# Kernel optimization log

Measured on AMD Instinct MI355X. Metric: run time of the kernel, lower is better.

The kernel has to match this reference:

```python
import jax, jax.numpy as jnp
import numpy as np

B, S, D, H = 8, 2048, 1024, 8
HD = D // H


def _linear_params(key, d_in, d_out):
    kw, kb = jax.random.split(key)
    w = jax.random.normal(kw, (d_out, d_in), jnp.float32) * 0.02
    b = jax.random.normal(kb, (d_out,), jnp.float32) * 0.02
    return w, b


def setup_inputs() -> dict:
    key = jax.random.key(0)
    ks = jax.random.split(key, 16)
    inp = {}
    inp['input_seq'] = jax.random.normal(ks[0], (B, S, D), jnp.float32)
    inp['output_seq'] = jax.random.normal(ks[1], (B, S, D), jnp.float32)
    # PositionalEncoding parameter: sin(arange(D) / 10000 ** (arange(D)/D))
    ar = jnp.arange(D, dtype=jnp.float32)
    inp['pe'] = jnp.sin(ar / 10000.0 ** (ar / D))
    names = ['enc_wq enc_bq', 'enc_wk enc_bk', 'enc_wv enc_bv',
             'enc_w1 enc_b1', 'enc_w2 enc_b2',
             'dec_s_wq dec_s_bq', 'dec_s_wk dec_s_bk', 'dec_s_wv dec_s_bv',
             'dec_c_wq dec_c_bq', 'dec_c_wk dec_c_bk', 'dec_c_wv dec_c_bv',
             'dec_w1 dec_b1', 'dec_w2 dec_b2', 'fc_w fc_b']
    for i, pair in enumerate(names):
        wn, bn = pair.split()
        w, b = _linear_params(ks[2 + i], D, D)
        inp[wn], inp[bn] = w, b
    return inp


def _mha(q_in, k_in, wq, bq, wk, bk, wv, bv):
    # Faithful to source: head split WITHOUT transpose -> per-position 8x8 head mixing.
    q = (q_in @ wq.T + bq).reshape(q_in.shape[0], q_in.shape[1], H, HD)
    k = (k_in @ wk.T + bk).reshape(k_in.shape[0], k_in.shape[1], H, HD)
    v = (k_in @ wv.T + bv).reshape(k_in.shape[0], k_in.shape[1], H, HD)
    scores = jnp.einsum('bsih,bsjh->bsij', q, k) / jnp.sqrt(jnp.float32(HD))
    w = jax.nn.softmax(scores, axis=-1)  # dropout before softmax is identity at eval
    out = jnp.einsum('bsij,bsjh->bsih', w, v)
    return out.reshape(q_in.shape[0], q_in.shape[1], -1)


def reference(input_seq, output_seq, pe,
              enc_wq, enc_bq, enc_wk, enc_bk, enc_wv, enc_bv,
              enc_w1, enc_b1, enc_w2, enc_b2,
              dec_s_wq, dec_s_bq, dec_s_wk, dec_s_bk, dec_s_wv, dec_s_bv,
              dec_c_wq, dec_c_bq, dec_c_wk, dec_c_bk, dec_c_wv, dec_c_bv,
              dec_w1, dec_b1, dec_w2, dec_b2, fc_w, fc_b):
    x = input_seq + pe  # additive positional encoding
    # encoder layer
    a = _mha(x, x, enc_wq, enc_bq, enc_wk, enc_bk, enc_wv, enc_bv)
    enc_out = jax.nn.relu(a @ enc_w1.T + enc_b1) @ enc_w2.T + enc_b2
    # decoder layer (training branch: output_seq given)
    sa = _mha(output_seq, output_seq, dec_s_wq, dec_s_bq, dec_s_wk, dec_s_bk, dec_s_wv, dec_s_bv)
    ca = _mha(sa, enc_out, dec_c_wq, dec_c_bq, dec_c_wk, dec_c_bk, dec_c_wv, dec_c_bv)
    dec_out = jax.nn.relu(ca @ dec_w1.T + dec_b1) @ dec_w2.T + dec_b2
    return dec_out @ fc_w.T + fc_b
```

## Files before the change

kernel.cpp:

```cpp
#include <hip/hip_runtime.h>
#include <stdint.h>


#define TOKENS 16384
#define DMODEL 1024

typedef unsigned short ushort_t;
typedef __attribute__((ext_vector_type(8))) short short8;
typedef __attribute__((ext_vector_type(4))) float floatx4;

__device__ __forceinline__ float b2f(ushort_t u) {
  union { uint32_t i; float f; } v; v.i = ((uint32_t)u) << 16; return v.f;
}
__device__ __forceinline__ ushort_t f2b(float f) {
  union { float f; uint32_t i; } v; v.f = f;
  uint32_t r = v.i + 0x7fffu + ((v.i >> 16) & 1u);
  return (ushort_t)(r >> 16);
}

__device__ __forceinline__ void pack8(const float* __restrict__ g, ushort_t* dst) {
  float4 x = *(const float4*)g;
  float4 y = *(const float4*)(g + 4);
  ushort_t o[8] = {f2b(x.x), f2b(x.y), f2b(x.z), f2b(x.w),
                   f2b(y.x), f2b(y.y), f2b(y.z), f2b(y.w)};
  *(uint4*)dst = *(uint4*)o;
}

#define GLD16(g, l)                                                          \
  __builtin_amdgcn_global_load_lds(                                          \
      (const __attribute__((address_space(1))) void*)(g),                    \
      (__attribute__((address_space(3))) void*)(l), 16, 0, 0)

struct ConvArgs {
  const float* src[14];
  ushort_t* dst[14];
};

__global__ __launch_bounds__(256) void conv_w_kernel(ConvArgs a) {
  const int w = blockIdx.y;
  const int idx = (blockIdx.x * 256 + threadIdx.x) * 8;
  pack8(a.src[w] + idx, a.dst[w] + idx);
}

__global__ __launch_bounds__(256) void conv_x_kernel(
    const float* __restrict__ src, ushort_t* __restrict__ dst) {
  const int idx = (blockIdx.x * 256 + threadIdx.x) * 8;
  pack8(src + idx, dst + idx);
}

__global__ __launch_bounds__(256) void add_pe_kernel(
    const float* __restrict__ in, const float* __restrict__ pe,
    ushort_t* __restrict__ out) {
  int idx = (blockIdx.x * 256 + threadIdx.x) * 8;
  int d = idx & (DMODEL - 1);
  float4 a0 = *(const float4*)(in + idx);
  float4 a1 = *(const float4*)(in + idx + 4);
  float4 p0 = *(const float4*)(pe + d);
  float4 p1 = *(const float4*)(pe + d + 4);
  ushort_t o[8] = {f2b(a0.x + p0.x), f2b(a0.y + p0.y), f2b(a0.z + p0.z), f2b(a0.w + p0.w),
                   f2b(a1.x + p1.x), f2b(a1.y + p1.y), f2b(a1.z + p1.z), f2b(a1.w + p1.w)};
  *(uint4*)(out + idx) = *(uint4*)o;
}

template <bool RELU, bool OUT32>
__global__ __launch_bounds__(256) void gemm_bt(
    const ushort_t* __restrict__ A, const ushort_t* __restrict__ W,
    const float* __restrict__ bias, void* __restrict__ Cp) {
  constexpr int K = 1024, N = 1024, BK = 64;
  __shared__ __align__(16) ushort_t smem[128 * 136];
  ushort_t* sA = smem;
  ushort_t* sB = smem + 8192;

  const int t = threadIdx.x;
  const int lane = t & 63;
  const int m0 = blockIdx.x * 128;
  const int n0 = blockIdx.y * 128;
  const int wm = ((t >> 6) >> 1) * 64;
  const int wn = ((t >> 6) & 1) * 64;

  floatx4 acc[4][4] = {};

  const int rl = t >> 3;
  const int j8 = t & 7;
  const ushort_t* gA = A + (size_t)(m0 + rl) * K + ((j8 ^ (rl & 7)) * 8);
  const ushort_t* gW = W + (size_t)(n0 + rl) * K + ((j8 ^ (rl & 7)) * 8);
  const int lo = t * 8;

  for (int k0 = 0; k0 < K; k0 += BK) {
#pragma unroll
    for (int s = 0; s < 4; s++) {
      GLD16(gA + k0 + (size_t)(s * 32) * K, sA + s * 2048 + lo);
      GLD16(gW + k0 + (size_t)(s * 32) * K, sB + s * 2048 + lo);
    }
    __syncthreads();

#pragma unroll
    for (int ks = 0; ks < 2; ks++) {
      short8 af[4], bf[4];
#pragma unroll
      for (int i = 0; i < 4; i++) {
        const int cs = ((ks * 4 + (lane >> 4)) ^ (lane & 7)) * 8;
        af[i] = *(const short8*)&sA[(wm + i * 16 + (lane & 15)) * 64 + cs];
        bf[i] = *(const short8*)&sB[(wn + i * 16 + (lane & 15)) * 64 + cs];
      }
#pragma unroll
      for (int i = 0; i < 4; i++)
#pragma unroll
        for (int jj = 0; jj < 4; jj++)
          acc[i][jj] = __builtin_amdgcn_mfma_f32_16x16x32_bf16(af[i], bf[jj], acc[i][jj], 0, 0, 0);
    }
    __syncthreads();
  }

  const int rbase = (lane >> 4) * 4;

  if (OUT32) {
    float* sCf = (float*)smem;
#pragma unroll
    for (int p = 0; p < 2; p++) {
      if (wm == p * 64) {
#pragma unroll
        for (int j = 0; j < 4; j++) {
          const int cl = wn + j * 16 + (lane & 15);
          const float bv = bias[n0 + cl];
#pragma unroll
          for (int i = 0; i < 4; i++)
#pragma unroll
            for (int r = 0; r < 4; r++) {
              float v = acc[i][j][r] + bv;
              if (RELU) v = fmaxf(v, 0.0f);
              sCf[(i * 16 + rbase + r) * 132 + cl] = v;
            }
        }
      }
      __syncthreads();
#pragma unroll
      for (int u = 0; u < 8; u++) {
        const int lin = u * 256 + t;
        const int row = lin >> 5;
        const int cc = (lin & 31) * 4;
        float4 v = *(const float4*)&sCf[row * 132 + cc];
        *(float4*)((float*)Cp + (size_t)(m0 + p * 64 + row) * N + n0 + cc) = v;
      }
      __syncthreads();
    }
    return;
  }

  ushort_t* sC = smem;
#pragma unroll
  for (int j = 0; j < 4; j++) {
    const int cl = wn + j * 16 + (lane & 15);
    const float bv = bias[n0 + cl];
#pragma unroll
    for (int i = 0; i < 4; i++) {
      const int rl2 = wm + i * 16 + rbase;
#pragma unroll
      for (int r = 0; r < 4; r++) {
        float v = acc[i][j][r] + bv;
        if (RELU) v = fmaxf(v, 0.0f);
        sC[(rl2 + r) * 136 + cl] = f2b(v);
      }
    }
  }
  __syncthreads();
#pragma unroll
  for (int p = 0; p < 8; p++) {
    const int rl2 = p * 16 + (t >> 4);
    const int cl = (t & 15) * 8;
    uint4 v = *(const uint4*)&sC[rl2 * 136 + cl];
    *(uint4*)((ushort_t*)Cp + (size_t)(m0 + rl2) * N + n0 + cl) = v;
  }
}

__global__ __launch_bounds__(256) void attn_kernel(
    const ushort_t* Q, const ushort_t* Kp, const ushort_t* Vp, ushort_t* O) {
  __shared__ __align__(16) ushort_t sq[4][1024];
  __shared__ __align__(16) ushort_t sk[4][1024];
  __shared__ __align__(16) ushort_t sv[4][1024];
  __shared__ float sp[4][64];

  const int t = threadIdx.x;
  const int w = t >> 6;
  const int lane = t & 63;
  const size_t base = ((size_t)blockIdx.x * 4 + w) * 1024;

  ((uint4*)sq[w])[lane] = ((const uint4*)(Q + base))[lane];
  ((uint4*)sq[w])[lane + 64] = ((const uint4*)(Q + base))[lane + 64];
  ((uint4*)sk[w])[lane] = ((const uint4*)(Kp + base))[lane];
  ((uint4*)sk[w])[lane + 64] = ((const uint4*)(Kp + base))[lane + 64];
  ((uint4*)sv[w])[lane] = ((const uint4*)(Vp + base))[lane];
  ((uint4*)sv[w])[lane + 64] = ((const uint4*)(Vp + base))[lane + 64];
  __syncthreads();

  {
    const int i = lane >> 3, j = lane & 7;
    const ushort_t* qr = &sq[w][i * 128];
    const ushort_t* kr = &sk[w][j * 128];
    float s = 0.0f;
#pragma unroll 16
    for (int h = 0; h < 128; h++) s += b2f(qr[h]) * b2f(kr[h]);
    s *= 0.08838834764831845f;
    float m = s;
#pragma unroll
    for (int off = 1; off < 8; off <<= 1) m = fmaxf(m, __shfl_xor(m, off, 64));
    float e = __expf(s - m);
    float sum = e;
#pragma unroll
    for (int off = 1; off < 8; off <<= 1) sum += __shfl_xor(sum, off, 64);
    sp[w][lane] = e / sum;
  }
  __syncthreads();

  {
    const int i = lane >> 3;
    const int hb = (lane & 7) * 16;
    float p[8];
#pragma unroll
    for (int jj = 0; jj < 8; jj++) p[jj] = sp[w][i * 8 + jj];
    float o[16];
#pragma unroll
    for (int h = 0; h < 16; h++) {
      float acc = 0.0f;
#pragma unroll
      for (int jj = 0; jj < 8; jj++) acc += p[jj] * b2f(sv[w][jj * 128 + hb + h]);
      o[h] = acc;
    }
    uint32_t packed[8];
#pragma unroll
    for (int u = 0; u < 8; u++)
      packed[u] = (uint32_t)f2b(o[2 * u]) | ((uint32_t)f2b(o[2 * u + 1]) << 16);
    uint4* dst = (uint4*)(O + base + i * 128 + hb);
    dst[0] = *(uint4*)&packed[0];
    dst[1] = *(uint4*)&packed[4];
  }
}

extern "C" void kernel_launch(void* const* d_in, const int* in_sizes, int n_in,
                              void* d_out, int out_size, void* d_ws, size_t ws_size,
                              hipStream_t stream) {
  const float* input_seq = (const float*)d_in[0];
  const float* output_seq = (const float*)d_in[1];
  const float* pe = (const float*)d_in[2];
  const float* wsrc[14] = {
      (const float*)d_in[3],  (const float*)d_in[5],  (const float*)d_in[7],
      (const float*)d_in[9],  (const float*)d_in[11], (const float*)d_in[13],
      (const float*)d_in[15], (const float*)d_in[17], (const float*)d_in[19],
      (const float*)d_in[21], (const float*)d_in[23], (const float*)d_in[25],
      (const float*)d_in[27], (const float*)d_in[29]};
  const float* enc_bq = (const float*)d_in[4];
  const float* enc_bk = (const float*)d_in[6];
  const float* enc_bv = (const float*)d_in[8];
  const float* enc_b1 = (const float*)d_in[10];
  const float* enc_b2 = (const float*)d_in[12];
  const float* dsq_b = (const float*)d_in[14];
  const float* dsk_b = (const float*)d_in[16];
  const float* dsv_b = (const float*)d_in[18];
  const float* dcq_b = (const float*)d_in[20];
  const float* dck_b = (const float*)d_in[22];
  const float* dcv_b = (const float*)d_in[24];
  const float* dec_b1 = (const float*)d_in[26];
  const float* dec_b2 = (const float*)d_in[28];
  const float* fc_b = (const float*)d_in[30];

  const size_t SZ = (size_t)TOKENS * DMODEL;
  const size_t WSZ = (size_t)DMODEL * DMODEL;
  ushort_t* bA = (ushort_t*)d_ws;
  ushort_t* bB = bA + SZ;
  ushort_t* oseq = bB + SZ;
  ushort_t* wts = oseq + SZ;
  ushort_t* oL = (ushort_t*)d_out;
  ushort_t* oH = oL + SZ;
  float* outf = (float*)d_out;

  ConvArgs ca;
#pragma unroll
  for (int i = 0; i < 14; i++) { ca.src[i] = wsrc[i]; ca.dst[i] = wts + (size_t)i * WSZ; }

  const dim3 gG(TOKENS / 128, DMODEL / 128);
  const dim3 blk(256);
  const int gPE = TOKENS * DMODEL / (256 * 8);
  const int gAT = TOKENS / 4;

  conv_w_kernel<<<dim3(WSZ / (256 * 8), 14), blk, 0, stream>>>(ca);
  conv_x_kernel<<<gPE, blk, 0, stream>>>(output_seq, oseq);
  add_pe_kernel<<<gPE, blk, 0, stream>>>(input_seq, pe, bA);
  gemm_bt<false, false><<<gG, blk, 0, stream>>>(bA, wts + 0 * WSZ, enc_bq, bB);
  gemm_bt<false, false><<<gG, blk, 0, stream>>>(bA, wts + 1 * WSZ, enc_bk, oL);
  gemm_bt<false, false><<<gG, blk, 0, stream>>>(bA, wts + 2 * WSZ, enc_bv, oH);
  attn_kernel<<<gAT, blk, 0, stream>>>(bB, oL, oH, bB);
  gemm_bt<true, false><<<gG, blk, 0, stream>>>(bB, wts + 3 * WSZ, enc_b1, bA);
  gemm_bt<false, false><<<gG, blk, 0, stream>>>(bA, wts + 4 * WSZ, enc_b2, bB);
  gemm_bt<false, false><<<gG, blk, 0, stream>>>(oseq, wts + 5 * WSZ, dsq_b, bA);
  gemm_bt<false, false><<<gG, blk, 0, stream>>>(oseq, wts + 6 * WSZ, dsk_b, oL);
  gemm_bt<false, false><<<gG, blk, 0, stream>>>(oseq, wts + 7 * WSZ, dsv_b, oH);
  attn_kernel<<<gAT, blk, 0, stream>>>(bA, oL, oH, bA);
  gemm_bt<false, false><<<gG, blk, 0, stream>>>(bA, wts + 8 * WSZ, dcq_b, oL);
  gemm_bt<false, false><<<gG, blk, 0, stream>>>(bB, wts + 9 * WSZ, dck_b, oH);
  gemm_bt<false, false><<<gG, blk, 0, stream>>>(bB, wts + 10 * WSZ, dcv_b, bA);
  attn_kernel<<<gAT, blk, 0, stream>>>(oL, oH, bA, oL);
  gemm_bt<true, false><<<gG, blk, 0, stream>>>(oL, wts + 11 * WSZ, dec_b1, bB);
  gemm_bt<false, false><<<gG, blk, 0, stream>>>(bB, wts + 12 * WSZ, dec_b2, bA);
  gemm_bt<false, true><<<gG, blk, 0, stream>>>(bA, wts + 13 * WSZ, fc_b, outf);
}
```

Measured before the change: 959.4 us.

## Rewrite GEMM as 256x256 tile, 8-wave, double-buffered ping-pong pipeline

Replaces the 128x128 single-buffered GEMM with a 256x256 tile computed by 512 threads. It double-buffers LDS (128KB dynamic) and interleaves global prefetch of the next K-tiles with quadrant-wise MFMA using explicit barriers, setprio and vmcnt waits. The block index is swizzled for L2 locality. This is meant to hide global load latency and raise data reuse per load, at the cost of heavy LDS use and fragile manual waitcnt scheduling.

```diff
diff --git a/kernel.cpp b/kernel.cpp
--- a/kernel.cpp
+++ b/kernel.cpp
@@ -62,85 +62,182 @@
   *(uint4*)(out + idx) = *(uint4*)o;
 }
 
+template <int D, int MH>
+__device__ __forceinline__ void load_a(const ushort_t* sA, int aoff, int cs0,
+                                       int cs1, short8 (&af)[4][2]) {
+  const ushort_t* p = sA + D * 16384 + MH * 8192 + aoff;
+#pragma unroll
+  for (int i = 0; i < 4; i++) {
+    af[i][0] = *(const short8*)&p[i * 1024 + cs0];
+    af[i][1] = *(const short8*)&p[i * 1024 + cs1];
+  }
+}
+
+template <int D, int NH>
+__device__ __forceinline__ void load_b(const ushort_t* sB, int boff, int cs0,
+                                       int cs1, short8 (&bf)[2][2]) {
+  const ushort_t* p = sB + D * 16384 + NH * 8192 + boff;
+#pragma unroll
+  for (int j = 0; j < 2; j++) {
+    bf[j][0] = *(const short8*)&p[j * 1024 + cs0];
+    bf[j][1] = *(const short8*)&p[j * 1024 + cs1];
+  }
+}
+
+template <int Q>
+__device__ __forceinline__ void mfma_q(floatx4 (&acc)[4][4][2],
+                                       const short8 (&af)[4][2],
+                                       const short8 (&bf)[2][2]) {
+  __builtin_amdgcn_s_setprio(1);
+#pragma unroll
+  for (int i = 0; i < 4; i++)
+#pragma unroll
+    for (int j = 0; j < 2; j++) {
+      acc[Q][i][j] = __builtin_amdgcn_mfma_f32_16x16x32_bf16(
+          af[i][0], bf[j][0], acc[Q][i][j], 0, 0, 0);
+      acc[Q][i][j] = __builtin_amdgcn_mfma_f32_16x16x32_bf16(
+          af[i][1], bf[j][1], acc[Q][i][j], 0, 0, 0);
+    }
+  __builtin_amdgcn_s_setprio(0);
+}
+
+#define BARSB                                                                \
+  do {                                                                       \
+    __builtin_amdgcn_s_barrier();                                            \
+    __builtin_amdgcn_sched_barrier(0);                                       \
+  } while (0)
+
+#define STAGE_A(h, tk, d)                                                    \
+  do {                                                                       \
+    GLD16(gA + (size_t)((h) * 131072 + (tk) * 64),                           \
+          sA + (d) * 16384 + (h) * 8192 + lo);                               \
+    GLD16(gA + (size_t)((h) * 131072 + 65536 + (tk) * 64),                   \
+          sA + (d) * 16384 + (h) * 8192 + 4096 + lo);                        \
+  } while (0)
+#define STAGE_B(h, tk, d)                                                    \
+  do {                                                                       \
+    GLD16(gB + (size_t)((h) * 131072 + (tk) * 64),                           \
+          sB + (d) * 16384 + (h) * 8192 + lo);                               \
+    GLD16(gB + (size_t)((h) * 131072 + 65536 + (tk) * 64),                   \
+          sB + (d) * 16384 + (h) * 8192 + 4096 + lo);                        \
+  } while (0)
+
+#define GROUP(tt, dd)                                                        \
+  do {                                                                       \
+    load_a<dd, 0>(sA, aoff, cs0, cs1, af);                                   \
+    load_b<dd, 0>(sB, boff, cs0, cs1, bf);                                   \
+    if ((tt) + 1 < NT) {                                                     \
+      STAGE_B(0, (tt) + 1, dd ^ 1);                                          \
+      STAGE_A(1, (tt) + 1, dd ^ 1);                                          \
+    }                                                                        \
+    BARSB;                                                                   \
+    mfma_q<0>(acc, af, bf);                                                  \
+    BARSB;                                                                   \
+    load_b<dd, 1>(sB, boff, cs0, cs1, bf);                                   \
+    BARSB;                                                                   \
+    mfma_q<1>(acc, af, bf);                                                  \
+    BARSB;                                                                   \
+    load_a<dd, 1>(sA, aoff, cs0, cs1, af);                                   \
+    if ((tt) + 2 < NT) STAGE_A(0, (tt) + 2, dd);                             \
+    BARSB;                                                                   \
+    mfma_q<3>(acc, af, bf);                                                  \
+    BARSB;                                                                   \
+    load_b<dd, 0>(sB, boff, cs0, cs1, bf);                                   \
+    if ((tt) + 2 < NT) STAGE_B(1, (tt) + 2, dd);                             \
+    BARSB;                                                                   \
+    mfma_q<2>(acc, af, bf);                                                  \
+    if ((tt) + 2 < NT) {                                                     \
+      asm volatile("s_waitcnt vmcnt(4)");                                    \
+    } else {                                                                 \
+      asm volatile("s_waitcnt vmcnt(0)");                                    \
+    }                                                                        \
+    BARSB;                                                                   \
+  } while (0)
+
 template <bool RELU, bool OUT32>
-__global__ __launch_bounds__(256) void gemm_bt(
+__global__ __launch_bounds__(512, 2) void gemm_bt(
     const ushort_t* __restrict__ A, const ushort_t* __restrict__ W,
     const float* __restrict__ bias, void* __restrict__ Cp) {
-  constexpr int K = 1024, N = 1024, BK = 64;
-  __shared__ __align__(16) ushort_t smem[128 * 136];
+  constexpr int K = 1024, N = 1024, NT = 16;
+  extern __shared__ ushort_t smem[];
   ushort_t* sA = smem;
-  ushort_t* sB = smem + 8192;
-
-  const int t = threadIdx.x;
-  const int lane = t & 63;
-  const int m0 = blockIdx.x * 128;
-  const int n0 = blockIdx.y * 128;
-  const int wm = ((t >> 6) >> 1) * 64;
-  const int wn = ((t >> 6) & 1) * 64;
-
-  floatx4 acc[4][4] = {};
-
-  const int rl = t >> 3;
-  const int j8 = t & 7;
-  const ushort_t* gA = A + (size_t)(m0 + rl) * K + ((j8 ^ (rl & 7)) * 8);
-  const ushort_t* gW = W + (size_t)(n0 + rl) * K + ((j8 ^ (rl & 7)) * 8);
-  const int lo = t * 8;
-
-  for (int k0 = 0; k0 < K; k0 += BK) {
-#pragma unroll
-    for (int s = 0; s < 4; s++) {
-      GLD16(gA + k0 + (size_t)(s * 32) * K, sA + s * 2048 + lo);
-      GLD16(gW + k0 + (size_t)(s * 32) * K, sB + s * 2048 + lo);
-    }
-    __syncthreads();
-
-#pragma unroll
-    for (int ks = 0; ks < 2; ks++) {
-      short8 af[4], bf[4];
-#pragma unroll
-      for (int i = 0; i < 4; i++) {
-        const int cs = ((ks * 4 + (lane >> 4)) ^ (lane & 7)) * 8;
-        af[i] = *(const short8*)&sA[(wm + i * 16 + (lane & 15)) * 64 + cs];
-        bf[i] = *(const short8*)&sB[(wn + i * 16 + (lane & 15)) * 64 + cs];
-      }
-#pragma unroll
-      for (int i = 0; i < 4; i++)
-#pragma unroll
-        for (int jj = 0; jj < 4; jj++)
-          acc[i][jj] = __builtin_amdgcn_mfma_f32_16x16x32_bf16(af[i], bf[jj], acc[i][jj], 0, 0, 0);
-    }
-    __syncthreads();
-  }
-
-  const int rbase = (lane >> 4) * 4;
-
-  if (OUT32) {
+  ushort_t* sB = smem + 32768;
+
+  const int tid = threadIdx.x;
+  const int lane = tid & 63;
+  const int wid = tid >> 6;
+
+  const int orig = blockIdx.x;
+  const int swz = (orig & 7) * 32 + (orig >> 3);
+  const int m0 = (swz >> 2) * 256;
+  const int n0 = (swz & 3) * 256;
+
+  const int qm = (wid >> 2) * 64;
+  const int qn = (wid & 3) * 32;
+  const int lr = lane & 15;
+  const int lq = lane >> 4;
+  const int xr = lane & 7;
+  const int cs0 = (lq ^ xr) * 8;
+  const int cs1 = ((4 + lq) ^ xr) * 8;
+  const int aoff = (qm + lr) * 64;
+  const int boff = (qn + lr) * 64;
+
+  const int rl = tid >> 3;
+  const int j8 = tid & 7;
+  const int co = (j8 ^ (rl & 7)) * 8;
+  const int lo = tid * 8;
+  const ushort_t* gA = A + (size_t)(m0 + rl) * K + co;
+  const ushort_t* gB = W + (size_t)(n0 + rl) * K + co;
+
+  floatx4 acc[4][4][2] = {};
+  short8 af[4][2], bf[2][2];
+
+  STAGE_A(0, 0, 0);
+  STAGE_B(1, 0, 0);
+  STAGE_B(0, 0, 0);
+  STAGE_A(1, 0, 0);
+  STAGE_A(0, 1, 1);
+  STAGE_B(1, 1, 1);
+  asm volatile("s_waitcnt vmcnt(4)");
+  BARSB;
+
+#pragma unroll 1
+  for (int t = 0; t < NT; t += 2) {
+    GROUP(t, 0);
+    GROUP(t + 1, 1);
+  }
+
+  const int rbase = lq * 4;
+
+  if constexpr (OUT32) {
     float* sCf = (float*)smem;
 #pragma unroll
-    for (int p = 0; p < 2; p++) {
-      if (wm == p * 64) {
-#pragma unroll
-        for (int j = 0; j < 4; j++) {
-          const int cl = wn + j * 16 + (lane & 15);
-          const float bv = bias[n0 + cl];
-#pragma unroll
-          for (int i = 0; i < 4; i++)
-#pragma unroll
-            for (int r = 0; r < 4; r++) {
-              float v = acc[i][j][r] + bv;
-              if (RELU) v = fmaxf(v, 0.0f);
-              sCf[(i * 16 + rbase + r) * 132 + cl] = v;
-            }
-        }
+    for (int p = 0; p < 4; p++) {
+      if ((qm >> 6) == (p & 1)) {
+#pragma unroll
+        for (int Nh = 0; Nh < 2; Nh++)
+#pragma unroll
+          for (int j = 0; j < 2; j++) {
+            const int col = Nh * 128 + qn + j * 16 + lr;
+            const float bv = bias[n0 + col];
+#pragma unroll
+            for (int i = 0; i < 4; i++)
+#pragma unroll
+              for (int r = 0; r < 4; r++) {
+                float v = acc[(p >> 1) * 2 + Nh][i][j][r] + bv;
+                if (RELU) v = fmaxf(v, 0.0f);
+                sCf[(i * 16 + rbase + r) * 260 + col] = v;
+              }
+          }
       }
       __syncthreads();
 #pragma unroll
       for (int u = 0; u < 8; u++) {
-        const int lin = u * 256 + t;
-        const int row = lin >> 5;
-        const int cc = (lin & 31) * 4;
-        float4 v = *(const float4*)&sCf[row * 132 + cc];
-        *(float4*)((float*)Cp + (size_t)(m0 + p * 64 + row) * N + n0 + cc) = v;
+        const int lin = u * 512 + tid;
+        const int row = lin >> 6;
+        const int c4 = (lin & 63) * 4;
+        *(float4*)((float*)Cp + (size_t)(m0 + p * 64 + row) * N + n0 + c4) =
+            *(const float4*)&sCf[row * 260 + c4];
       }
       __syncthreads();
     }
@@ -149,27 +246,32 @@
 
   ushort_t* sC = smem;
 #pragma unroll
-  for (int j = 0; j < 4; j++) {
-    const int cl = wn + j * 16 + (lane & 15);
-    const float bv = bias[n0 + cl];
-#pragma unroll
-    for (int i = 0; i < 4; i++) {
-      const int rl2 = wm + i * 16 + rbase;
-#pragma unroll
-      for (int r = 0; r < 4; r++) {
-        float v = acc[i][j][r] + bv;
-        if (RELU) v = fmaxf(v, 0.0f);
-        sC[(rl2 + r) * 136 + cl] = f2b(v);
+  for (int p = 0; p < 2; p++) {
+#pragma unroll
+    for (int Nh = 0; Nh < 2; Nh++)
+#pragma unroll
+      for (int j = 0; j < 2; j++) {
+        const int col = Nh * 128 + qn + j * 16 + lr;
+        const float bv = bias[n0 + col];
+#pragma unroll
+        for (int i = 0; i < 4; i++)
+#pragma unroll
+          for (int r = 0; r < 4; r++) {
+            float v = acc[p * 2 + Nh][i][j][r] + bv;
+            if (RELU) v = fmaxf(v, 0.0f);
+            sC[(qm + i * 16 + rbase + r) * 264 + col] = f2b(v);
+          }
       }
+    __syncthreads();
+#pragma unroll
+    for (int u = 0; u < 8; u++) {
+      const int lin = u * 512 + tid;
+      const int row = lin >> 5;
+      const int c8 = (lin & 31) * 8;
+      *(uint4*)((ushort_t*)Cp + (size_t)(m0 + p * 128 + row) * N + n0 + c8) =
+          *(const uint4*)&sC[row * 264 + c8];
     }
-  }
-  __syncthreads();
-#pragma unroll
-  for (int p = 0; p < 8; p++) {
-    const int rl2 = p * 16 + (t >> 4);
-    const int cl = (t & 15) * 8;
-    uint4 v = *(const uint4*)&sC[rl2 * 136 + cl];
-    *(uint4*)((ushort_t*)Cp + (size_t)(m0 + rl2) * N + n0 + cl) = v;
+    __syncthreads();
   }
 }
 
@@ -273,33 +375,46 @@
   ushort_t* oH = oL + SZ;
   float* outf = (float*)d_out;
 
+  static bool attr_set = false;
+  if (!attr_set) {
+    (void)hipFuncSetAttribute(reinterpret_cast<const void*>(&gemm_bt<false, false>),
+                              hipFuncAttributeMaxDynamicSharedMemorySize, 131072);
+    (void)hipFuncSetAttribute(reinterpret_cast<const void*>(&gemm_bt<true, false>),
+                              hipFuncAttributeMaxDynamicSharedMemorySize, 131072);
+    (void)hipFuncSetAttribute(reinterpret_cast<const void*>(&gemm_bt<false, true>),
+                              hipFuncAttributeMaxDynamicSharedMemorySize, 131072);
+    attr_set = true;
+  }
+
   ConvArgs ca;
 #pragma unroll
   for (int i = 0; i < 14; i++) { ca.src[i] = wsrc[i]; ca.dst[i] = wts + (size_t)i * WSZ; }
 
-  const dim3 gG(TOKENS / 128, DMODEL / 128);
+  const dim3 gG(TOKENS / 256 * (DMODEL / 256));
+  const dim3 gblk(512);
   const dim3 blk(256);
+  const int LDSB = 131072;
   const int gPE = TOKENS * DMODEL / (256 * 8);
   const int gAT = TOKENS / 4;
 
   conv_w_kernel<<<dim3(WSZ / (256 * 8), 14), blk, 0, stream>>>(ca);
   conv_x_kernel<<<gPE, blk, 0, stream>>>(output_seq, oseq);
   add_pe_kernel<<<gPE, blk, 0, stream>>>(input_seq, pe, bA);
-  gemm_bt<false, false><<<gG, blk, 0, stream>>>(bA, wts + 0 * WSZ, enc_bq, bB);
-  gemm_bt<false, false><<<gG, blk, 0, stream>>>(bA, wts + 1 * WSZ, enc_bk, oL);
-  gemm_bt<false, false><<<gG, blk, 0, stream>>>(bA, wts + 2 * WSZ, enc_bv, oH);
+  gemm_bt<false, false><<<gG, gblk, LDSB, stream>>>(bA, wts + 0 * WSZ, enc_bq, bB);
+  gemm_bt<false, false><<<gG, gblk, LDSB, stream>>>(bA, wts + 1 * WSZ, enc_bk, oL);
+  gemm_bt<false, false><<<gG, gblk, LDSB, stream>>>(bA, wts + 2 * WSZ, enc_bv, oH);
   attn_kernel<<<gAT, blk, 0, stream>>>(bB, oL, oH, bB);
-  gemm_bt<true, false><<<gG, blk, 0, stream>>>(bB, wts + 3 * WSZ, enc_b1, bA);
-  gemm_bt<false, false><<<gG, blk, 0, stream>>>(bA, wts + 4 * WSZ, enc_b2, bB);
-  gemm_bt<false, false><<<gG, blk, 0, stream>>>(oseq, wts + 5 * WSZ, dsq_b, bA);
-  gemm_bt<false, false><<<gG, blk, 0, stream>>>(oseq, wts + 6 * WSZ, dsk_b, oL);
-  gemm_bt<false, false><<<gG, blk, 0, stream>>>(oseq, wts + 7 * WSZ, dsv_b, oH);
+  gemm_bt<true, false><<<gG, gblk, LDSB, stream>>>(bB, wts + 3 * WSZ, enc_b1, bA);
+  gemm_bt<false, false><<<gG, gblk, LDSB, stream>>>(bA, wts + 4 * WSZ, enc_b2, bB);
+  gemm_bt<false, false><<<gG, gblk, LDSB, stream>>>(oseq, wts + 5 * WSZ, dsq_b, bA);
+  gemm_bt<false, false><<<gG, gblk, LDSB, stream>>>(oseq, wts + 6 * WSZ, dsk_b, oL);
+  gemm_bt<false, false><<<gG, gblk, LDSB, stream>>>(oseq, wts + 7 * WSZ, dsv_b, oH);
   attn_kernel<<<gAT, blk, 0, stream>>>(bA, oL, oH, bA);
-  gemm_bt<false, false><<<gG, blk, 0, stream>>>(bA, wts + 8 * WSZ, dcq_b, oL);
-  gemm_bt<false, false><<<gG, blk, 0, stream>>>(bB, wts + 9 * WSZ, dck_b, oH);
-  gemm_bt<false, false><<<gG, blk, 0, stream>>>(bB, wts + 10 * WSZ, dcv_b, bA);
+  gemm_bt<false, false><<<gG, gblk, LDSB, stream>>>(bA, wts + 8 * WSZ, dcq_b, oL);
+  gemm_bt<false, false><<<gG, gblk, LDSB, stream>>>(bB, wts + 9 * WSZ, dck_b, oH);
+  gemm_bt<false, false><<<gG, gblk, LDSB, stream>>>(bB, wts + 10 * WSZ, dcv_b, bA);
   attn_kernel<<<gAT, blk, 0, stream>>>(oL, oH, bA, oL);
-  gemm_bt<true, false><<<gG, blk, 0, stream>>>(oL, wts + 11 * WSZ, dec_b1, bB);
-  gemm_bt<false, false><<<gG, blk, 0, stream>>>(bB, wts + 12 * WSZ, dec_b2, bA);
-  gemm_bt<false, true><<<gG, blk, 0, stream>>>(bA, wts + 13 * WSZ, fc_b, outf);
-}
+  gemm_bt<true, false><<<gG, gblk, LDSB, stream>>>(oL, wts + 11 * WSZ, dec_b1, bB);
+  gemm_bt<false, false><<<gG, gblk, LDSB, stream>>>(bB, wts + 12 * WSZ, dec_b2, bA);
+  gemm_bt<false, true><<<gG, gblk, LDSB, stream>>>(bA, wts + 13 * WSZ, fc_b, outf);
+}
```

New measurement: 832.3 us. -13.2%, faster.
